# Optimization experiments

Measured on AMD Instinct MI355X. Metric: run time of the kernel, lower is better.

## Reference

```python
import jax, jax.numpy as jnp
import numpy as np

NUM_HEADS = 12


def setup_inputs() -> dict:
    key = jax.random.key(0)
    ks = jax.random.split(key, 5)
    B, N, C = 4, 2048, 768
    s = 0.02
    return {
        "x": jax.random.normal(ks[0], (B, N, C), jnp.float32),
        "qkv_w": jax.random.normal(ks[1], (3 * C, C), jnp.float32) * s,
        "qkv_b": jax.random.normal(ks[2], (3 * C,), jnp.float32) * s,
        "proj_w": jax.random.normal(ks[3], (C, C), jnp.float32) * s,
        "proj_b": jax.random.normal(ks[4], (C,), jnp.float32) * s,
    }


def reference(x, qkv_w, qkv_b, proj_w, proj_b):
    B, N, C = x.shape
    H = NUM_HEADS
    D = C // H
    scale = D ** -0.5
    # qkv projection: [B,N,3C] -> [3,B,H,N,D]
    qkv = (x @ qkv_w.T + qkv_b).reshape(B, N, 3, H, D).transpose(2, 0, 3, 1, 4)
    q, k, v = qkv[0], qkv[1], qkv[2]
    attn = jnp.einsum("bhnd,bhmd->bhnm", q, k) * scale  # [B,H,N,N]
    attn_probs = jax.nn.softmax(attn, axis=-1)
    # dropout p=0 (eval) -> identity
    out = jnp.einsum("bhnm,bhmd->bhnd", attn_probs, v)  # [B,H,N,D]
    out = out.transpose(0, 2, 1, 3).reshape(B, N, C)
    return out @ proj_w.T + proj_b
```

## Files before the change

kernel.cpp:

```cpp
#include <hip/hip_runtime.h>

typedef __attribute__((ext_vector_type(8))) short bf16x8;
typedef __attribute__((ext_vector_type(4))) float f32x4;
typedef __attribute__((ext_vector_type(4))) unsigned int u32x4;

#define QSCALE 0.1803368801111243f

__device__ inline unsigned short f2bf(float f) {
  union { float f; unsigned u; } v; v.f = f;
  unsigned r = v.u + 0x7fffu + ((v.u >> 16) & 1u);
  return (unsigned short)(r >> 16);
}

__device__ inline unsigned packbf2(float a, float b) {
  union { float f; unsigned u; } va, vb; va.f = a; vb.f = b;
  unsigned ta = va.u + 0x7fffu + ((va.u >> 16) & 1u);
  unsigned tb = vb.u + 0x7fffu + ((vb.u >> 16) & 1u);
  return __builtin_amdgcn_perm(tb, ta, 0x07060302);
}

__device__ inline void async16(const void* g, void* l) {
  __builtin_amdgcn_global_load_lds(
      (const __attribute__((address_space(1))) unsigned int*)g,
      (__attribute__((address_space(3))) unsigned int*)l, 16, 0, 0);
}


__device__ inline void swz_one(const float* __restrict__ src, unsigned short* __restrict__ dst,
                               int idx) {
  int l16 = idx & 15, quad = (idx >> 4) & 3, mi = (idx >> 6) & 3;
  int rest = idx >> 8;
  int cg = rest % 24, g = rest / 24;
  int row = g * 64 + mi * 16 + l16;
  int k = cg * 32 + quad * 8;
  const float* s = src + (size_t)row * 768 + k;
  float4 v0 = *(const float4*)s, v1 = *(const float4*)(s + 4);
  u32x4 o;
  o.x = packbf2(v0.x, v0.y); o.y = packbf2(v0.z, v0.w);
  o.z = packbf2(v1.x, v1.y); o.w = packbf2(v1.z, v1.w);
  *(u32x4*)(dst + (size_t)idx * 8) = o;
}

__global__ __launch_bounds__(256) void swz_x(const float* __restrict__ x,
                                             unsigned short* __restrict__ xs) {
  swz_one(x, xs, blockIdx.x * 256 + threadIdx.x);
}

__global__ __launch_bounds__(256) void swz_w(const float* __restrict__ wq,
                                             const float* __restrict__ wp,
                                             unsigned short* __restrict__ wqs,
                                             unsigned short* __restrict__ wps) {
  int idx = blockIdx.x * 256 + threadIdx.x;
  if (idx < 221184) swz_one(wq, wqs, idx);
  else              swz_one(wp, wps, idx - 221184);
}

template<int MODE>
__global__ __launch_bounds__(256, MODE == 0 ? 3 : 4) void gemm_swz(
    const unsigned short* __restrict__ A, const unsigned short* __restrict__ B,
    const float* __restrict__ bias,
    unsigned short* __restrict__ oq, unsigned short* __restrict__ ok,
    unsigned short* __restrict__ ov, float* __restrict__ of)
{
  constexpr int NI = (MODE == 0) ? 4 : 2;
  const int t = threadIdx.x, w = t >> 6, lane = t & 63;
  const int quad = lane >> 4, l16 = lane & 15;
  const int bm = blockIdx.x, bn = blockIdx.y;

  const int gA = (MODE == 0) ? (bm * 2 + (w >> 1)) : bm;
  const unsigned short* Ab = A + (size_t)gA * 49152 + (size_t)lane * 8;

  const unsigned short* Bb[NI];
#pragma unroll
  for (int ni = 0; ni < NI; ni++) {
    int n_base = bn * 128 + ((MODE == 0) ? (w & 1) * 64 : w * 32) + ni * 16;
    Bb[ni] = B + (size_t)(n_base >> 6) * 49152 + (size_t)((n_base >> 4) & 3) * 512
               + (size_t)lane * 8;
  }

  f32x4 acc[4][NI] = {};
  bf16x8 af[2][4], bf_[2][NI];

#pragma unroll
  for (int mi = 0; mi < 4; mi++) af[0][mi] = *(const bf16x8*)(Ab + mi * 512);
#pragma unroll
  for (int ni = 0; ni < NI; ni++) bf_[0][ni] = *(const bf16x8*)(Bb[ni]);

#pragma unroll
  for (int cg = 0; cg < 24; cg++) {
    const int cur = cg & 1;
    if (cg < 23) {
#pragma unroll
      for (int mi = 0; mi < 4; mi++)
        af[cur ^ 1][mi] = *(const bf16x8*)(Ab + (cg + 1) * 2048 + mi * 512);
#pragma unroll
      for (int ni = 0; ni < NI; ni++)
        bf_[cur ^ 1][ni] = *(const bf16x8*)(Bb[ni] + (cg + 1) * 2048);
    }
#pragma unroll
    for (int mi = 0; mi < 4; mi++)
#pragma unroll
      for (int ni = 0; ni < NI; ni++)
        acc[mi][ni] = __builtin_amdgcn_mfma_f32_16x16x32_bf16(af[cur][mi], bf_[cur][ni],
                                                              acc[mi][ni], 0, 0, 0);
  }

  if (MODE == 0) {
    const int three = (bn * 128) / 768;
#pragma unroll
    for (int ni = 0; ni < NI; ni++) {
      int n_g = bn * 128 + (w & 1) * 64 + ni * 16 + l16;
      float bs = bias[n_g];
      int rem = n_g - three * 768;
      int h = rem >> 6, d = rem & 63;
#pragma unroll
      for (int mi = 0; mi < 4; mi++) {
#pragma unroll
        for (int r = 0; r < 4; r++) {
          int m_g = gA * 64 + mi * 16 + (quad << 2) + r;
          int b_ = m_g >> 11, ntok = m_g & 2047;
          float v = acc[mi][ni][r] + bs;
          if (three == 0)
            oq[(((size_t)b_ * 12 + h) * 2048 + ntok) * 64 + d] = f2bf(v * QSCALE);
          else if (three == 1)
            ok[(((size_t)b_ * 12 + h) * 2048 + ntok) * 64 + d] = f2bf(v);
          else
            ov[(((size_t)b_ * 12 + h) * 64 + d) * 2048 + ntok] = f2bf(v);
        }
      }
    }
  } else {
#pragma unroll
    for (int ni = 0; ni < NI; ni++) {
      int n_g = bn * 128 + w * 32 + ni * 16 + l16;
      float bs = bias[n_g];
#pragma unroll
      for (int mi = 0; mi < 4; mi++) {
#pragma unroll
        for (int r = 0; r < 4; r++) {
          int m_g = bm * 64 + mi * 16 + (quad << 2) + r;
          of[(size_t)m_g * 768 + n_g] = acc[mi][ni][r] + bs;
        }
      }
    }
  }
}

__global__ __launch_bounds__(256, 3) void flash_attn(
    const unsigned short* __restrict__ Qb, const unsigned short* __restrict__ Kb,
    const unsigned short* __restrict__ Vtb, unsigned short* __restrict__ aos)
{
  __shared__ unsigned short Ks[2][4096];
  __shared__ unsigned short Vs[2][4096];
  const int t = threadIdx.x, w = t >> 6, lane = t & 63;
  const int quad = lane >> 4, l16 = lane & 15;
  const int bh = blockIdx.x, qt = blockIdx.y;
  const unsigned short* Qg = Qb + (size_t)bh * 2048 * 64;
  const unsigned short* Kg = Kb + (size_t)bh * 2048 * 64;
  const unsigned short* Vg = Vtb + (size_t)bh * 2048 * 64;

  bf16x8 bq[2][2];
#pragma unroll
  for (int u = 0; u < 2; u++) {
    int qrow = qt * 128 + w * 32 + u * 16 + l16;
#pragma unroll
    for (int h = 0; h < 2; h++)
      bq[u][h] = *(const bf16x8*)(Qg + (size_t)qrow * 64 + h * 32 + quad * 8);
  }

  const int s0 = t, s1 = 256 + t;
  auto gperm = [](int s) { return (s & 0x23) | ((s & 0x0c) << 1) | ((s & 0x10) >> 2); };
  const size_t koff0 = (size_t)gperm(s0 & 63) * 64 + (s0 >> 6) * 8;
  const size_t koff1 = (size_t)gperm(s1 & 63) * 64 + (s1 >> 6) * 8;
  const size_t voff0 = (size_t)(s0 & 63) * 2048 + (s0 >> 6) * 8;
  const size_t voff1 = (size_t)(s1 & 63) * 2048 + (s1 >> 6) * 8;

  float l_run[2] = {0.f, 0.f};
  f32x4 o_acc[2][4];
#pragma unroll
  for (int u = 0; u < 2; u++)
#pragma unroll
    for (int dt = 0; dt < 4; dt++) o_acc[u][dt] = (f32x4){0.f, 0.f, 0.f, 0.f};

  async16(Kg + koff0, &Ks[0][s0 * 8]);
  async16(Kg + koff1, &Ks[0][s1 * 8]);
  async16(Vg + voff0, &Vs[0][s0 * 8]);
  async16(Vg + voff1, &Vs[0][s1 * 8]);

  for (int kt = 0; kt < 32; kt++) {
    const int p = kt & 1;
    __syncthreads();
    if (kt < 31) {
      const unsigned short* Kn = Kg + (size_t)(kt + 1) * 4096;
      const unsigned short* Vn = Vg + (size_t)(kt + 1) * 64;
      async16(Kn + koff0, &Ks[p ^ 1][s0 * 8]);
      async16(Kn + koff1, &Ks[p ^ 1][s1 * 8]);
      async16(Vn + voff0, &Vs[p ^ 1][s0 * 8]);
      async16(Vn + voff1, &Vs[p ^ 1][s1 * 8]);
    }
    const unsigned short* Kp = &Ks[p][0];
    const unsigned short* Vp = &Vs[p][0];

    f32x4 sv[2][4];
#pragma unroll
    for (int nt = 0; nt < 4; nt++) {
      bf16x8 k0 = *(const bf16x8*)&Kp[((quad) * 64 + nt * 16 + l16) * 8];
      bf16x8 k1 = *(const bf16x8*)&Kp[((4 + quad) * 64 + nt * 16 + l16) * 8];
#pragma unroll
      for (int u = 0; u < 2; u++) {
        f32x4 s_ = {0.f, 0.f, 0.f, 0.f};
        s_ = __builtin_amdgcn_mfma_f32_16x16x32_bf16(k0, bq[u][0], s_, 0, 0, 0);
        s_ = __builtin_amdgcn_mfma_f32_16x16x32_bf16(k1, bq[u][1], s_, 0, 0, 0);
        sv[u][nt] = s_;
      }
    }

    union { unsigned u32[8]; bf16x8 v[2]; } pk[2];
#pragma unroll
    for (int u = 0; u < 2; u++) {
#pragma unroll
      for (int nt = 0; nt < 4; nt++) {
        float p0 = __builtin_amdgcn_exp2f(sv[u][nt][0]);
        float p1 = __builtin_amdgcn_exp2f(sv[u][nt][1]);
        float p2 = __builtin_amdgcn_exp2f(sv[u][nt][2]);
        float p3 = __builtin_amdgcn_exp2f(sv[u][nt][3]);
        l_run[u] += (p0 + p1) + (p2 + p3);
        pk[u].u32[nt * 2]     = packbf2(p0, p1);
        pk[u].u32[nt * 2 + 1] = packbf2(p2, p3);
      }
    }

#pragma unroll
    for (int cc = 0; cc < 2; cc++) {
#pragma unroll
      for (int dt = 0; dt < 4; dt++) {
        bf16x8 a = *(const bf16x8*)&Vp[((cc * 4 + quad) * 64 + dt * 16 + l16) * 8];
#pragma unroll
        for (int u = 0; u < 2; u++)
          o_acc[u][dt] = __builtin_amdgcn_mfma_f32_16x16x32_bf16(a, pk[u].v[cc], o_acc[u][dt], 0, 0, 0);
      }
    }
  }

  float linv[2];
#pragma unroll
  for (int u = 0; u < 2; u++) {
    float l = l_run[u];
    l += __shfl_xor(l, 16, 64);
    l += __shfl_xor(l, 32, 64);
    linv[u] = 1.f / l;
  }

  const int b_ = bh / 12, h = bh - b_ * 12;
  const int g_ = b_ * 32 + qt * 2 + (w >> 1);
#pragma unroll
  for (int u = 0; u < 2; u++) {
    const int mi = (w * 2 + u) & 3;
    unsigned short* base = aos + (size_t)g_ * 49152 + mi * 512 + l16 * 8;
#pragma unroll
    for (int dt = 0; dt < 4; dt++) {
      int cg = h * 2 + (dt >> 1);
      int cq = (dt & 1) * 2 + (quad >> 1);
#pragma unroll
      for (int pr = 0; pr < 2; pr++) {
        float v0 = o_acc[u][dt][pr * 2] * linv[u];
        float v1 = o_acc[u][dt][pr * 2 + 1] * linv[u];
        int j = (quad & 1) * 4 + pr * 2;
        *(unsigned*)(base + cg * 2048 + cq * 128 + j) = packbf2(v0, v1);
      }
    }
  }
}

extern "C" void kernel_launch(void* const* d_in, const int* in_sizes, int n_in,
                              void* d_out, int out_size, void* d_ws, size_t ws_size,
                              hipStream_t stream) {
  const float* x      = (const float*)d_in[0];
  const float* qkv_w  = (const float*)d_in[1];
  const float* qkv_b  = (const float*)d_in[2];
  const float* proj_w = (const float*)d_in[3];
  const float* proj_b = (const float*)d_in[4];
  float* out = (float*)d_out;

  unsigned short* ws  = (unsigned short*)d_ws;
  unsigned short* wqs = ws;
  unsigned short* wps = wqs + 1769472;
  unsigned short* xs  = wps + 589824;
  unsigned short* qb  = xs + 6291456;
  unsigned short* kb  = qb + 6291456;
  unsigned short* vtb = kb + 6291456;
  unsigned short* aos = vtb + 6291456;

  swz_w<<<1152, 256, 0, stream>>>(qkv_w, proj_w, wqs, wps);
  swz_x<<<3072, 256, 0, stream>>>(x, xs);
  gemm_swz<0><<<dim3(64, 18), 256, 0, stream>>>(xs, wqs, qkv_b, qb, kb, vtb, nullptr);
  flash_attn<<<dim3(48, 16), 256, 0, stream>>>(qb, kb, vtb, aos);
  gemm_swz<1><<<dim3(128, 6), 256, 0, stream>>>(aos, wps, proj_b, nullptr, nullptr, nullptr, out);
}
```

Before: 237.2 us.

## Rework QKV GEMM with LDS tiling, plain casts, larger attention and proj tiles

Replaces the swizzled x/weight pre-pass with a plain bf16 cast and adds a new 256x128 LDS-staged QKV GEMM using 512-thread blocks. The output projection now uses 128x128 tiles (64x6 grid). Flash attention moves to 512 threads covering 256 query rows, so each K/V tile staged in LDS serves more queries and each thread issues one async load per tile. The aim is more data reuse and fewer blocks, at the cost of extra barriers in the GEMM and fewer blocks in flight, which can lower occupancy.

After: 305.7 us. 28.9% more time.

```diff
diff --git a/kernel.cpp b/kernel.cpp
--- a/kernel.cpp
+++ b/kernel.cpp
@@ -25,66 +25,157 @@
       (__attribute__((address_space(3))) unsigned int*)l, 16, 0, 0);
 }
 
-
-__device__ inline void swz_one(const float* __restrict__ src, unsigned short* __restrict__ dst,
-                               int idx) {
+__global__ __launch_bounds__(256) void cast_plain(
+    const float* __restrict__ x, const float* __restrict__ wq,
+    unsigned short* __restrict__ xb, unsigned short* __restrict__ wqb)
+{
+  long i = (long)blockIdx.x * 256 + threadIdx.x;
+  const float* src; unsigned short* dst;
+  if (i < 1572864L) { src = x + i * 4; dst = xb + i * 4; }
+  else              { long j = i - 1572864L; src = wq + j * 4; dst = wqb + j * 4; }
+  float4 v = *(const float4*)src;
+  uint2 o;
+  o.x = packbf2(v.x, v.y);
+  o.y = packbf2(v.z, v.w);
+  *(uint2*)dst = o;
+}
+
+__global__ __launch_bounds__(256) void swz_wp(const float* __restrict__ wp,
+                                              unsigned short* __restrict__ wps) {
+  int idx = blockIdx.x * 256 + threadIdx.x;
   int l16 = idx & 15, quad = (idx >> 4) & 3, mi = (idx >> 6) & 3;
   int rest = idx >> 8;
   int cg = rest % 24, g = rest / 24;
   int row = g * 64 + mi * 16 + l16;
   int k = cg * 32 + quad * 8;
-  const float* s = src + (size_t)row * 768 + k;
+  const float* s = wp + (size_t)row * 768 + k;
   float4 v0 = *(const float4*)s, v1 = *(const float4*)(s + 4);
   u32x4 o;
   o.x = packbf2(v0.x, v0.y); o.y = packbf2(v0.z, v0.w);
   o.z = packbf2(v1.x, v1.y); o.w = packbf2(v1.z, v1.w);
-  *(u32x4*)(dst + (size_t)idx * 8) = o;
-}
-
-__global__ __launch_bounds__(256) void swz_x(const float* __restrict__ x,
-                                             unsigned short* __restrict__ xs) {
-  swz_one(x, xs, blockIdx.x * 256 + threadIdx.x);
-}
-
-__global__ __launch_bounds__(256) void swz_w(const float* __restrict__ wq,
-                                             const float* __restrict__ wp,
-                                             unsigned short* __restrict__ wqs,
-                                             unsigned short* __restrict__ wps) {
-  int idx = blockIdx.x * 256 + threadIdx.x;
-  if (idx < 221184) swz_one(wq, wqs, idx);
-  else              swz_one(wp, wps, idx - 221184);
-}
-
-template<int MODE>
-__global__ __launch_bounds__(256, MODE == 0 ? 3 : 4) void gemm_swz(
-    const unsigned short* __restrict__ A, const unsigned short* __restrict__ B,
+  *(u32x4*)(wps + (size_t)idx * 8) = o;
+}
+
+__global__ __launch_bounds__(512) void gemm_qkv(
+    const unsigned short* __restrict__ A, const unsigned short* __restrict__ Bt,
     const float* __restrict__ bias,
     unsigned short* __restrict__ oq, unsigned short* __restrict__ ok,
-    unsigned short* __restrict__ ov, float* __restrict__ of)
+    unsigned short* __restrict__ ov)
 {
-  constexpr int NI = (MODE == 0) ? 4 : 2;
+  constexpr int K = 768;
+  __shared__ unsigned short As[16384];
+  __shared__ unsigned short Bs[8192];
+  const int t = threadIdx.x;
+  const int w = t >> 6, lane = t & 63;
+  const int quad = lane >> 4, l16 = lane & 15;
+  const int bm = blockIdx.x, bn = blockIdx.y;
+  const int wm = (w >> 1) << 6, wn = (w & 1) << 6;
+
+  f32x4 acc[4][4] = {};
+
+  const unsigned short* Ag = A + (size_t)bm * 256 * K;
+  const unsigned short* Bg = Bt + (size_t)bn * 128 * K;
+
+  const unsigned short* abase[4];
+  const unsigned short* bbase[2];
+#pragma unroll
+  for (int i = 0; i < 4; i++) {
+    int s = i * 512 + t;
+    abase[i] = Ag + (size_t)(s & 255) * K + (s >> 8) * 8;
+  }
+#pragma unroll
+  for (int i = 0; i < 2; i++) {
+    int s = i * 512 + t;
+    bbase[i] = Bg + (size_t)(s & 127) * K + (s >> 7) * 8;
+  }
+
+  u32x4 ra[4], rb[2];
+  auto fetch = [&](int k0) {
+#pragma unroll
+    for (int i = 0; i < 4; i++) ra[i] = *(const u32x4*)(abase[i] + k0);
+#pragma unroll
+    for (int i = 0; i < 2; i++) rb[i] = *(const u32x4*)(bbase[i] + k0);
+  };
+
+  fetch(0);
+
+#pragma unroll
+  for (int it = 0; it < K / 64; it++) {
+    __syncthreads();
+#pragma unroll
+    for (int i = 0; i < 4; i++) *(u32x4*)&As[(i * 512 + t) * 8] = ra[i];
+#pragma unroll
+    for (int i = 0; i < 2; i++) *(u32x4*)&Bs[(i * 512 + t) * 8] = rb[i];
+    __syncthreads();
+    if (it < K / 64 - 1) fetch((it + 1) * 64);
+
+#pragma unroll
+    for (int kk = 0; kk < 2; kk++) {
+      bf16x8 a[4], b[4];
+#pragma unroll
+      for (int mi = 0; mi < 4; mi++)
+        a[mi] = *(const bf16x8*)&As[(((kk << 2) + quad) * 256 + wm + (mi << 4) + l16) * 8];
+#pragma unroll
+      for (int ni = 0; ni < 4; ni++)
+        b[ni] = *(const bf16x8*)&Bs[(((kk << 2) + quad) * 128 + wn + (ni << 4) + l16) * 8];
+#pragma unroll
+      for (int mi = 0; mi < 4; mi++)
+#pragma unroll
+        for (int ni = 0; ni < 4; ni++)
+          acc[mi][ni] = __builtin_amdgcn_mfma_f32_16x16x32_bf16(a[mi], b[ni], acc[mi][ni], 0, 0, 0);
+    }
+  }
+
+  const int three = (bn * 128) / 768;
+#pragma unroll
+  for (int ni = 0; ni < 4; ni++) {
+    int n_g = bn * 128 + wn + (ni << 4) + l16;
+    float bs = bias[n_g];
+    int rem = n_g - three * 768;
+    int h = rem >> 6, d = rem & 63;
+#pragma unroll
+    for (int mi = 0; mi < 4; mi++) {
+#pragma unroll
+      for (int r = 0; r < 4; r++) {
+        int m_g = bm * 256 + wm + (mi << 4) + (quad << 2) + r;
+        int b_ = m_g >> 11, ntok = m_g & 2047;
+        float v = acc[mi][ni][r] + bs;
+        if (three == 0)
+          oq[(((size_t)b_ * 12 + h) * 2048 + ntok) * 64 + d] = f2bf(v * QSCALE);
+        else if (three == 1)
+          ok[(((size_t)b_ * 12 + h) * 2048 + ntok) * 64 + d] = f2bf(v);
+        else
+          ov[(((size_t)b_ * 12 + h) * 64 + d) * 2048 + ntok] = f2bf(v);
+      }
+    }
+  }
+}
+
+__global__ __launch_bounds__(256) void gemm_proj(
+    const unsigned short* __restrict__ A, const unsigned short* __restrict__ B,
+    const float* __restrict__ bias, float* __restrict__ of)
+{
   const int t = threadIdx.x, w = t >> 6, lane = t & 63;
   const int quad = lane >> 4, l16 = lane & 15;
   const int bm = blockIdx.x, bn = blockIdx.y;
 
-  const int gA = (MODE == 0) ? (bm * 2 + (w >> 1)) : bm;
+  const int gA = bm * 2 + (w >> 1);
   const unsigned short* Ab = A + (size_t)gA * 49152 + (size_t)lane * 8;
 
-  const unsigned short* Bb[NI];
-#pragma unroll
-  for (int ni = 0; ni < NI; ni++) {
-    int n_base = bn * 128 + ((MODE == 0) ? (w & 1) * 64 : w * 32) + ni * 16;
+  const unsigned short* Bb[4];
+#pragma unroll
+  for (int ni = 0; ni < 4; ni++) {
+    int n_base = bn * 128 + (w & 1) * 64 + ni * 16;
     Bb[ni] = B + (size_t)(n_base >> 6) * 49152 + (size_t)((n_base >> 4) & 3) * 512
                + (size_t)lane * 8;
   }
 
-  f32x4 acc[4][NI] = {};
-  bf16x8 af[2][4], bf_[2][NI];
-
+  f32x4 acc[4][4] = {};
+  bf16x8 af[2][4], bf_[2][4];
 #pragma unroll
   for (int mi = 0; mi < 4; mi++) af[0][mi] = *(const bf16x8*)(Ab + mi * 512);
 #pragma unroll
-  for (int ni = 0; ni < NI; ni++) bf_[0][ni] = *(const bf16x8*)(Bb[ni]);
+  for (int ni = 0; ni < 4; ni++) bf_[0][ni] = *(const bf16x8*)(Bb[ni]);
 
 #pragma unroll
   for (int cg = 0; cg < 24; cg++) {
@@ -94,59 +185,33 @@
       for (int mi = 0; mi < 4; mi++)
         af[cur ^ 1][mi] = *(const bf16x8*)(Ab + (cg + 1) * 2048 + mi * 512);
 #pragma unroll
-      for (int ni = 0; ni < NI; ni++)
+      for (int ni = 0; ni < 4; ni++)
         bf_[cur ^ 1][ni] = *(const bf16x8*)(Bb[ni] + (cg + 1) * 2048);
     }
 #pragma unroll
     for (int mi = 0; mi < 4; mi++)
 #pragma unroll
-      for (int ni = 0; ni < NI; ni++)
+      for (int ni = 0; ni < 4; ni++)
         acc[mi][ni] = __builtin_amdgcn_mfma_f32_16x16x32_bf16(af[cur][mi], bf_[cur][ni],
                                                               acc[mi][ni], 0, 0, 0);
   }
 
-  if (MODE == 0) {
-    const int three = (bn * 128) / 768;
-#pragma unroll
-    for (int ni = 0; ni < NI; ni++) {
-      int n_g = bn * 128 + (w & 1) * 64 + ni * 16 + l16;
-      float bs = bias[n_g];
-      int rem = n_g - three * 768;
-      int h = rem >> 6, d = rem & 63;
-#pragma unroll
-      for (int mi = 0; mi < 4; mi++) {
-#pragma unroll
-        for (int r = 0; r < 4; r++) {
-          int m_g = gA * 64 + mi * 16 + (quad << 2) + r;
-          int b_ = m_g >> 11, ntok = m_g & 2047;
-          float v = acc[mi][ni][r] + bs;
-          if (three == 0)
-            oq[(((size_t)b_ * 12 + h) * 2048 + ntok) * 64 + d] = f2bf(v * QSCALE);
-          else if (three == 1)
-            ok[(((size_t)b_ * 12 + h) * 2048 + ntok) * 64 + d] = f2bf(v);
-          else
-            ov[(((size_t)b_ * 12 + h) * 64 + d) * 2048 + ntok] = f2bf(v);
-        }
-      }
-    }
-  } else {
-#pragma unroll
-    for (int ni = 0; ni < NI; ni++) {
-      int n_g = bn * 128 + w * 32 + ni * 16 + l16;
-      float bs = bias[n_g];
-#pragma unroll
-      for (int mi = 0; mi < 4; mi++) {
-#pragma unroll
-        for (int r = 0; r < 4; r++) {
-          int m_g = bm * 64 + mi * 16 + (quad << 2) + r;
-          of[(size_t)m_g * 768 + n_g] = acc[mi][ni][r] + bs;
-        }
-      }
-    }
-  }
-}
-
-__global__ __launch_bounds__(256, 3) void flash_attn(
+#pragma unroll
+  for (int ni = 0; ni < 4; ni++) {
+    int n_g = bn * 128 + (w & 1) * 64 + ni * 16 + l16;
+    float bs = bias[n_g];
+#pragma unroll
+    for (int mi = 0; mi < 4; mi++) {
+#pragma unroll
+      for (int r = 0; r < 4; r++) {
+        int m_g = gA * 64 + mi * 16 + (quad << 2) + r;
+        of[(size_t)m_g * 768 + n_g] = acc[mi][ni][r] + bs;
+      }
+    }
+  }
+}
+
+__global__ __launch_bounds__(512) void flash_attn(
     const unsigned short* __restrict__ Qb, const unsigned short* __restrict__ Kb,
     const unsigned short* __restrict__ Vtb, unsigned short* __restrict__ aos)
 {
@@ -162,18 +227,15 @@
   bf16x8 bq[2][2];
 #pragma unroll
   for (int u = 0; u < 2; u++) {
-    int qrow = qt * 128 + w * 32 + u * 16 + l16;
+    int qrow = qt * 256 + w * 32 + u * 16 + l16;
 #pragma unroll
     for (int h = 0; h < 2; h++)
       bq[u][h] = *(const bf16x8*)(Qg + (size_t)qrow * 64 + h * 32 + quad * 8);
   }
 
-  const int s0 = t, s1 = 256 + t;
   auto gperm = [](int s) { return (s & 0x23) | ((s & 0x0c) << 1) | ((s & 0x10) >> 2); };
-  const size_t koff0 = (size_t)gperm(s0 & 63) * 64 + (s0 >> 6) * 8;
-  const size_t koff1 = (size_t)gperm(s1 & 63) * 64 + (s1 >> 6) * 8;
-  const size_t voff0 = (size_t)(s0 & 63) * 2048 + (s0 >> 6) * 8;
-  const size_t voff1 = (size_t)(s1 & 63) * 2048 + (s1 >> 6) * 8;
+  const size_t koff = (size_t)gperm(t & 63) * 64 + (t >> 6) * 8;
+  const size_t voff = (size_t)(t & 63) * 2048 + (t >> 6) * 8;
 
   float l_run[2] = {0.f, 0.f};
   f32x4 o_acc[2][4];
@@ -182,21 +244,15 @@
 #pragma unroll
     for (int dt = 0; dt < 4; dt++) o_acc[u][dt] = (f32x4){0.f, 0.f, 0.f, 0.f};
 
-  async16(Kg + koff0, &Ks[0][s0 * 8]);
-  async16(Kg + koff1, &Ks[0][s1 * 8]);
-  async16(Vg + voff0, &Vs[0][s0 * 8]);
-  async16(Vg + voff1, &Vs[0][s1 * 8]);
+  async16(Kg + koff, &Ks[0][t * 8]);
+  async16(Vg + voff, &Vs[0][t * 8]);
 
   for (int kt = 0; kt < 32; kt++) {
     const int p = kt & 1;
     __syncthreads();
     if (kt < 31) {
-      const unsigned short* Kn = Kg + (size_t)(kt + 1) * 4096;
-      const unsigned short* Vn = Vg + (size_t)(kt + 1) * 64;
-      async16(Kn + koff0, &Ks[p ^ 1][s0 * 8]);
-      async16(Kn + koff1, &Ks[p ^ 1][s1 * 8]);
-      async16(Vn + voff0, &Vs[p ^ 1][s0 * 8]);
-      async16(Vn + voff1, &Vs[p ^ 1][s1 * 8]);
+      async16(Kg + (size_t)(kt + 1) * 4096 + koff, &Ks[p ^ 1][t * 8]);
+      async16(Vg + (size_t)(kt + 1) * 64 + voff, &Vs[p ^ 1][t * 8]);
     }
     const unsigned short* Kp = &Ks[p][0];
     const unsigned short* Vp = &Vs[p][0];
@@ -252,10 +308,11 @@
   }
 
   const int b_ = bh / 12, h = bh - b_ * 12;
-  const int g_ = b_ * 32 + qt * 2 + (w >> 1);
 #pragma unroll
   for (int u = 0; u < 2; u++) {
-    const int mi = (w * 2 + u) & 3;
+    const int wu = w * 2 + u;
+    const int g_ = b_ * 32 + qt * 4 + (wu >> 2);
+    const int mi = wu & 3;
     unsigned short* base = aos + (size_t)g_ * 49152 + mi * 512 + l16 * 8;
 #pragma unroll
     for (int dt = 0; dt < 4; dt++) {
@@ -283,17 +340,17 @@
   float* out = (float*)d_out;
 
   unsigned short* ws  = (unsigned short*)d_ws;
-  unsigned short* wqs = ws;
-  unsigned short* wps = wqs + 1769472;
-  unsigned short* xs  = wps + 589824;
-  unsigned short* qb  = xs + 6291456;
+  unsigned short* xb  = ws;
+  unsigned short* wqb = xb + 6291456;
+  unsigned short* wps = wqb + 1769472;
+  unsigned short* qb  = wps + 589824;
   unsigned short* kb  = qb + 6291456;
   unsigned short* vtb = kb + 6291456;
   unsigned short* aos = vtb + 6291456;
 
-  swz_w<<<1152, 256, 0, stream>>>(qkv_w, proj_w, wqs, wps);
-  swz_x<<<3072, 256, 0, stream>>>(x, xs);
-  gemm_swz<0><<<dim3(64, 18), 256, 0, stream>>>(xs, wqs, qkv_b, qb, kb, vtb, nullptr);
-  flash_attn<<<dim3(48, 16), 256, 0, stream>>>(qb, kb, vtb, aos);
-  gemm_swz<1><<<dim3(128, 6), 256, 0, stream>>>(aos, wps, proj_b, nullptr, nullptr, nullptr, out);
-}
+  cast_plain<<<7872, 256, 0, stream>>>(x, qkv_w, xb, wqb);
+  swz_wp<<<288, 256, 0, stream>>>(proj_w, wps);
+  gemm_qkv<<<dim3(32, 18), 512, 0, stream>>>(xb, wqb, qkv_b, qb, kb, vtb);
+  flash_attn<<<dim3(48, 8), 512, 0, stream>>>(qb, kb, vtb, aos);
+  gemm_proj<<<dim3(64, 6), 256, 0, stream>>>(aos, wps, proj_b, out);
+}
```
